# Performance work log

Hardware: AMD Instinct MI355X
Metric: run time of the kernel (lower is better)

Reference implementation:

```python
import jax, jax.numpy as jnp
from jax import lax
import numpy as np

EPS = 1e-5


def fps(xyz, npoint):
    # farthest point sampling, starts at index 0 (pointnet2 convention). xyz: (B,N,3)
    B, N, _ = xyz.shape
    def step(carry, _):
        dist, last = carry
        lastp = jnp.take_along_axis(xyz, last[:, None, None], axis=1)  # (B,1,3)
        d2 = jnp.sum((xyz - lastp) ** 2, axis=-1)                      # (B,N)
        dist = jnp.minimum(dist, d2)
        nxt = jnp.argmax(dist, axis=-1).astype(jnp.int32)
        return (dist, nxt), last
    init = (jnp.full((B, N), 1e10, xyz.dtype), jnp.zeros((B,), jnp.int32))
    _, idxs = lax.scan(step, init, None, length=npoint)
    return jnp.transpose(idxs)  # (B, npoint)


def gather2(x, idx):
    # x (B,N,C), idx (B,S) -> (B,S,C)
    return jnp.take_along_axis(x, idx[..., None], axis=1)


def gather3(x, idx):
    # x (B,N,C), idx (B,S,K) -> (B,S,K,C)
    return jnp.take_along_axis(x[:, None], idx[..., None], axis=2)


def ball_query(xyz, new_xyz, radius, nsample):
    # first nsample indices (in original point order) within radius; pad with first hit
    d2 = jnp.sum((new_xyz[:, :, None, :] - xyz[:, None, :, :]) ** 2, axis=-1)  # (B,S,N)
    N = xyz.shape[1]
    mask = d2 < radius * radius
    cand = jnp.where(mask, jnp.arange(N, dtype=jnp.int32), N)
    cand = jnp.sort(cand, axis=-1)[..., :nsample]
    first = cand[..., :1]
    cand = jnp.where(cand == N, first, cand)
    return jnp.where(cand == N, 0, cand)


def shared_mlp(h, layers):
    # h: (B,S,K,C); 1x1 conv == per-point linear; BN2d with batch stats; ReLU
    for W, g, b in layers:
        h = jnp.einsum('bskc,cd->bskd', h, W)
        mu = jnp.mean(h, axis=(0, 1, 2))
        var = jnp.var(h, axis=(0, 1, 2))
        h = jax.nn.relu((h - mu) * lax.rsqrt(var + EPS) * g + b)
    return h


def sa_module(xyz, feat, npoint, radius, nsample, layers):
    if npoint is None:  # group-all
        grouped = jnp.concatenate([xyz, feat], axis=-1)[:, None]  # (B,1,N,3+C)
        new_xyz = xyz[:, :1]
    else:
        cidx = fps(xyz, npoint)
        new_xyz = gather2(xyz, cidx)                              # (B,S,3)
        nidx = ball_query(xyz, new_xyz, radius, nsample)          # (B,S,K)
        gxyz = gather3(xyz, nidx) - new_xyz[:, :, None, :]        # centered xyz
        grouped = jnp.concatenate([gxyz, gather3(feat, nidx)], axis=-1)
    return new_xyz, jnp.max(shared_mlp(grouped, layers), axis=2)  # (B,S,D)


def bn1d_relu(x, g, b):
    mu = jnp.mean(x, axis=0)
    var = jnp.var(x, axis=0)
    return jax.nn.relu((x - mu) * lax.rsqrt(var + EPS) * g + b)


def setup_inputs():
    key = jax.random.key(0)
    ks = jax.random.split(key, 16)
    B, NP, NG = 64, 1024, 256
    inp = {}
    # points in a 0.1-side cube so radius-0.02/0.04 balls contain realistic neighbor counts
    inp['pc'] = jax.random.uniform(ks[0], (B, NP, 3), jnp.float32) * 0.1
    inp['gripper_pc'] = jax.random.uniform(ks[1], (B, NG, 3), jnp.float32) * 0.1
    def conv(k, cin, cout):
        return jax.random.normal(k, (cin, cout), jnp.float32) * (1.0 / np.sqrt(cin))
    specs = {'w1a': (7, 64), 'w1b': (64, 64), 'w1c': (64, 128),
             'w2a': (131, 128), 'w2b': (128, 128), 'w2c': (128, 256),
             'w3a': (259, 256), 'w3b': (256, 256), 'w3c': (256, 512)}
    i = 2
    for name, (cin, cout) in specs.items():
        inp[name] = conv(ks[i], cin, cout); i += 1
        inp['g' + name[1:]] = jnp.ones((cout,), jnp.float32)
        inp['b' + name[1:]] = jnp.zeros((cout,), jnp.float32)
    inp['fw1'] = conv(ks[i], 512, 1024); i += 1
    inp['fb1'] = jnp.zeros((1024,), jnp.float32)
    inp['fg1'] = jnp.ones((1024,), jnp.float32)
    inp['fbb1'] = jnp.zeros((1024,), jnp.float32)
    inp['fw2'] = conv(ks[i], 1024, 1024); i += 1
    inp['fb2'] = jnp.zeros((1024,), jnp.float32)
    inp['fg2'] = jnp.ones((1024,), jnp.float32)
    inp['fbb2'] = jnp.zeros((1024,), jnp.float32)
    inp['hw'] = conv(ks[i], 1024, 1); i += 1
    inp['hb'] = jnp.zeros((1,), jnp.float32)
    return inp


def reference(pc, gripper_pc,
              w1a, g1a, b1a, w1b, g1b, b1b, w1c, g1c, b1c,
              w2a, g2a, b2a, w2b, g2b, b2b, w2c, g2c, b2c,
              w3a, g3a, b3a, w3b, g3b, b3b, w3c, g3c, b3c,
              fw1, fb1, fg1, fbb1, fw2, fb2, fg2, fbb2, hw, hb):
    B, NP, _ = pc.shape
    NG = gripper_pc.shape[1]
    xyz = jnp.concatenate([pc, gripper_pc], axis=1)                       # (B,N,3)
    labels = jnp.concatenate([jnp.ones((B, NP, 1), pc.dtype),
                              jnp.zeros((B, NG, 1), pc.dtype)], axis=1)
    feat = jnp.concatenate([xyz, labels], axis=-1)                        # (B,N,4)
    xyz, feat = sa_module(xyz, feat, 128, 0.02, 64,
                          [(w1a, g1a, b1a), (w1b, g1b, b1b), (w1c, g1c, b1c)])
    xyz, feat = sa_module(xyz, feat, 32, 0.04, 128,
                          [(w2a, g2a, b2a), (w2b, g2b, b2b), (w2c, g2c, b2c)])
    _, feat = sa_module(xyz, feat, None, None, None,
                        [(w3a, g3a, b3a), (w3b, g3b, b3b), (w3c, g3c, b3c)])
    x = feat[:, 0]                                                        # (B,512)
    x = bn1d_relu(x @ fw1 + fb1, fg1, fbb1)
    x = bn1d_relu(x @ fw2 + fb2, fg2, fbb2)
    return x @ hw + hb                                                    # (B,1) logits
```

## Files before the change

### kernel.cpp

```cpp
#include <hip/hip_runtime.h>

#define BN_EPS 1e-5f
#define MFMA_B16(a, b, c) __builtin_amdgcn_mfma_f32_16x16x32_bf16((a), (b), (c), 0, 0, 0)

typedef short s16x8 __attribute__((ext_vector_type(8)));
typedef float f32x4v __attribute__((ext_vector_type(4)));

__device__ __forceinline__ unsigned fenc(float f) {
    unsigned u = __float_as_uint(f);
    return (u & 0x80000000u) ? ~u : (u | 0x80000000u);
}
__device__ __forceinline__ float fdec(unsigned e) {
    unsigned u = (e & 0x80000000u) ? (e ^ 0x80000000u) : ~e;
    return __uint_as_float(u);
}
__device__ __forceinline__ unsigned short f2b(float f) {
    unsigned u = __float_as_uint(f);
    unsigned r = u + 0x7FFFu + ((u >> 16) & 1u);
    return (unsigned short)(r >> 16);
}
__device__ __forceinline__ float b2f(unsigned short h) {
    return __uint_as_float(((unsigned)h) << 16);
}

__device__ __forceinline__ void cmb(float& v, int& i, float ov, int oi) {
    bool t = (ov > v) || ((ov == v) && (oi < i));
    v = t ? ov : v;
    i = t ? oi : i;
}
template<int CTRL>
__device__ __forceinline__ float dppf(float x) {
    return __uint_as_float((unsigned)__builtin_amdgcn_update_dpp(
        0, (int)__float_as_uint(x), CTRL, 0xF, 0xF, true));
}
template<int CTRL>
__device__ __forceinline__ int dppi(int x) {
    return __builtin_amdgcn_update_dpp(0, x, CTRL, 0xF, 0xF, true);
}

__global__ __launch_bounds__(256) void build_xyz_kernel(
    const float* __restrict__ pc, const float* __restrict__ gpc, float* __restrict__ xyz)
{
    int p = blockIdx.x * 256 + threadIdx.x;
    if (p >= 64 * 1280) return;
    int b = p / 1280, i = p % 1280;
    const float* src = (i < 1024) ? (pc + ((size_t)b * 1024 + i) * 3)
                                  : (gpc + ((size_t)b * 256 + (i - 1024)) * 3);
    xyz[(size_t)p * 3 + 0] = src[0];
    xyz[(size_t)p * 3 + 1] = src[1];
    xyz[(size_t)p * 3 + 2] = src[2];
}

__global__ __launch_bounds__(256) void prep_w_kernel(
    const float* __restrict__ w2a, const float* __restrict__ w2b, const float* __restrict__ w2c,
    const float* __restrict__ w1a, const float* __restrict__ w1b, const float* __restrict__ w1c,
    unsigned short* __restrict__ W1Th, unsigned short* __restrict__ W1Tl,
    unsigned short* __restrict__ W2Th, unsigned short* __restrict__ W2Tl,
    unsigned short* __restrict__ W3Th, unsigned short* __restrict__ W3Tl,
    unsigned short* __restrict__ A1Th, unsigned short* __restrict__ A1Tl,
    unsigned short* __restrict__ B1Th, unsigned short* __restrict__ B1Tl,
    unsigned short* __restrict__ C1Th, unsigned short* __restrict__ C1Tl)
{
    int i = blockIdx.x * 256 + threadIdx.x;
    float v = 0.f;
    unsigned short* dh; unsigned short* dl; int j;
    if (i < 20480) {
        int n = i / 160, k = i % 160;
        if (k < 128)       v = w2a[(size_t)(3 + k) * 128 + n];
        else if (k < 131)  v = w2a[(size_t)(k - 128) * 128 + n];
        dh = W1Th; dl = W1Tl; j = i;
    } else if (i < 36864) {
        j = i - 20480;
        int n = j / 128, k = j % 128;
        v = w2b[(size_t)k * 128 + n];
        dh = W2Th; dl = W2Tl;
    } else if (i < 69632) {
        j = i - 36864;
        int n = j / 128, k = j % 128;
        v = w2c[(size_t)k * 256 + n];
        dh = W3Th; dl = W3Tl;
    } else if (i < 71680) {
        j = i - 69632;
        int n = j / 32, k = j % 32;
        if (k < 7) v = w1a[(size_t)k * 64 + n];
        dh = A1Th; dl = A1Tl;
    } else if (i < 75776) {
        j = i - 71680;
        int n = j / 64, k = j % 64;
        v = w1b[(size_t)k * 64 + n];
        dh = B1Th; dl = B1Tl;
    } else if (i < 83968) {
        j = i - 75776;
        int n = j / 64, k = j % 64;
        v = w1c[(size_t)k * 128 + n];
        dh = C1Th; dl = C1Tl;
    } else return;
    unsigned short hi = f2b(v);
    unsigned short lo = f2b(v - b2f(hi));
    dh[j] = hi; dl[j] = lo;
}

__global__ __launch_bounds__(256) void reduce_stats_kernel(
    const float* __restrict__ PS, const float* __restrict__ PQ,
    int nblk, int C, float* __restrict__ osum, float* __restrict__ osq)
{
    __shared__ float rs_[256], rq_[256];
    int c = blockIdx.x, t = threadIdx.x;
    float s = 0.f, q = 0.f;
    for (int i = t; i < nblk; i += 256) {
        s += PS[(size_t)i * C + c];
        q += PQ[(size_t)i * C + c];
    }
    rs_[t] = s; rq_[t] = q;
    __syncthreads();
    for (int off = 128; off >= 1; off >>= 1) {
        if (t < off) { rs_[t] += rs_[t + off]; rq_[t] += rq_[t + off]; }
        __syncthreads();
    }
    if (t == 0) { osum[c] = rs_[0]; osq[c] = rq_[0]; }
}

template<int P>
__global__ __launch_bounds__(256, 1) void fps_mw_kernel(
    const float* __restrict__ xyz, int N, int S, int* __restrict__ oidx)
{
    __shared__ float sx[1280 * 3];
    __shared__ float rv[2][4];
    __shared__ int   ri[2][4];
    int b = blockIdx.x, t = threadIdx.x;
    int wv = t >> 6, lane = t & 63;
    for (int i = t; i < N * 3; i += 256) sx[i] = xyz[(size_t)b * N * 3 + i];
    __syncthreads();
    float px[P], py[P], pz[P], dm[P];
    #pragma unroll
    for (int p = 0; p < P; p++) {
        int i = t * P + p;
        px[p] = sx[i * 3]; py[p] = sx[i * 3 + 1]; pz[p] = sx[i * 3 + 2];
        dm[p] = 1e10f;
    }
    int last = 0;
    float lx = sx[0], ly = sx[1], lz = sx[2];
    for (int j = 0; j < S; j++) {
        if (t == 0) oidx[b * S + j] = last;
        float bestv = -1.f; int besti = 0;
        #pragma unroll
        for (int p = 0; p < P; p++) {
            float dx = px[p] - lx, dy = py[p] - ly, dz = pz[p] - lz;
            float d2 = __fadd_rn(__fadd_rn(__fmul_rn(dx, dx), __fmul_rn(dy, dy)), __fmul_rn(dz, dz));
            float d = fminf(dm[p], d2); dm[p] = d;
            if (d > bestv) { bestv = d; besti = t * P + p; }
        }
        cmb(bestv, besti, dppf<0xB1>(bestv),  dppi<0xB1>(besti));
        cmb(bestv, besti, dppf<0x4E>(bestv),  dppi<0x4E>(besti));
        cmb(bestv, besti, dppf<0x141>(bestv), dppi<0x141>(besti));
        cmb(bestv, besti, dppf<0x140>(bestv), dppi<0x140>(besti));
        cmb(bestv, besti, __shfl_xor(bestv, 16, 64), __shfl_xor(besti, 16, 64));
        cmb(bestv, besti, __shfl_xor(bestv, 32, 64), __shfl_xor(besti, 32, 64));
        if (lane == 0) { rv[j & 1][wv] = bestv; ri[j & 1][wv] = besti; }
        __syncthreads();
        float bv = rv[j & 1][0]; int bi = ri[j & 1][0];
        cmb(bv, bi, rv[j & 1][1], ri[j & 1][1]);
        cmb(bv, bi, rv[j & 1][2], ri[j & 1][2]);
        cmb(bv, bi, rv[j & 1][3], ri[j & 1][3]);
        last = bi;
        lx = sx[last * 3]; ly = sx[last * 3 + 1]; lz = sx[last * 3 + 2];
    }
}

template<int P>
__global__ __launch_bounds__(64, 1) void fps_wave_kernel(
    const float* __restrict__ xyz, int N, int S, int* __restrict__ oidx)
{
    __shared__ float sx[1280 * 3];
    int b = blockIdx.x, lane = threadIdx.x;
    for (int i = lane; i < N * 3; i += 64) sx[i] = xyz[(size_t)b * N * 3 + i];
    __syncthreads();
    float px[P], py[P], pz[P], dm[P];
    #pragma unroll
    for (int p = 0; p < P; p++) {
        int i = lane * P + p;
        px[p] = sx[i * 3]; py[p] = sx[i * 3 + 1]; pz[p] = sx[i * 3 + 2];
        dm[p] = 1e10f;
    }
    int last = 0;
    float lx = sx[0], ly = sx[1], lz = sx[2];
    for (int j = 0; j < S; j++) {
        if (lane == 0) oidx[b * S + j] = last;
        float bv0 = -1.f, bv1 = -1.f; int bi0 = 0, bi1 = 0;
        #pragma unroll
        for (int p = 0; p < P; p++) {
            float dx = px[p] - lx, dy = py[p] - ly, dz = pz[p] - lz;
            float d2 = __fadd_rn(__fadd_rn(__fmul_rn(dx, dx), __fmul_rn(dy, dy)), __fmul_rn(dz, dz));
            float d = fminf(dm[p], d2); dm[p] = d;
            if (p & 1) { if (d > bv1) { bv1 = d; bi1 = lane * P + p; } }
            else       { if (d > bv0) { bv0 = d; bi0 = lane * P + p; } }
        }
        float bestv = bv0; int besti = bi0;
        cmb(bestv, besti, bv1, bi1);
        cmb(bestv, besti, dppf<0xB1>(bestv),  dppi<0xB1>(besti));
        cmb(bestv, besti, dppf<0x4E>(bestv),  dppi<0x4E>(besti));
        cmb(bestv, besti, dppf<0x141>(bestv), dppi<0x141>(besti));
        cmb(bestv, besti, dppf<0x140>(bestv), dppi<0x140>(besti));
        cmb(bestv, besti, __shfl_xor(bestv, 16, 64), __shfl_xor(besti, 16, 64));
        cmb(bestv, besti, __shfl_xor(bestv, 32, 64), __shfl_xor(besti, 32, 64));
        last = besti;
        lx = sx[last * 3]; ly = sx[last * 3 + 1]; lz = sx[last * 3 + 2];
    }
}

__global__ __launch_bounds__(256) void ball_query_kernel(
    const float* __restrict__ xyz, const int* __restrict__ cidx,
    int N, int S, int nsample, float r2,
    int* __restrict__ nidx, float* __restrict__ newxyz)
{
    __shared__ float sx[1280 * 3];
    int b = blockIdx.x, t = threadIdx.x;
    for (int i = t; i < N * 3; i += 256) sx[i] = xyz[(size_t)b * N * 3 + i];
    __syncthreads();
    int w = t >> 6, lane = t & 63;
    int s = blockIdx.y * 4 + w;
    if (s >= S) return;
    int c = cidx[b * S + s];
    float cx = sx[c * 3], cy = sx[c * 3 + 1], cz = sx[c * 3 + 2];
    if (lane == 0) {
        newxyz[((size_t)b * S + s) * 3 + 0] = cx;
        newxyz[((size_t)b * S + s) * 3 + 1] = cy;
        newxyz[((size_t)b * S + s) * 3 + 2] = cz;
    }
    int P = N >> 6;
    int base = lane * P;
    unsigned mask = 0;
    for (int p = 0; p < P; p++) {
        int i = base + p;
        float dx = sx[i * 3] - cx, dy = sx[i * 3 + 1] - cy, dz = sx[i * 3 + 2] - cz;
        float d2 = __fadd_rn(__fadd_rn(__fmul_rn(dx, dx), __fmul_rn(dy, dy)), __fmul_rn(dz, dz));
        if (d2 < r2) mask |= (1u << p);
    }
    int cnt = __popc(mask);
    int pre = cnt;
    for (int off = 1; off < 64; off <<= 1) {
        int v = __shfl_up(pre, off, 64);
        if (lane >= off) pre += v;
    }
    int excl = pre - cnt;
    int total = __shfl(pre, 63, 64);
    size_t outb = ((size_t)b * S + s) * (size_t)nsample;
    unsigned mm = mask; int pos = excl;
    while (mm) {
        int p = __ffs(mm) - 1; mm &= mm - 1;
        if (pos < nsample) nidx[outb + pos] = base + p;
        pos++;
    }
    unsigned long long bal = __ballot(cnt > 0);
    int firstlane = __ffsll(bal) - 1;
    int firstidx = base + __ffs(mask) - 1;
    firstidx = __shfl(firstidx, firstlane, 64);
    for (int p = total + lane; p < nsample; p += 64) nidx[outb + p] = firstidx;
}

__global__ __launch_bounds__(256) void sa1_moment_kernel(
    const float* __restrict__ xyz, const int* __restrict__ nidx,
    const float* __restrict__ nx, float* __restrict__ mom)
{
    float a[35];
    #pragma unroll
    for (int i = 0; i < 35; i++) a[i] = 0.f;
    int gid = blockIdx.x * 256 + threadIdx.x;
    for (int ch = 0; ch < 8; ch++) {
        int r = ch * 65536 + gid;
        int n = nidx[r];
        int bs = r >> 6, b = r >> 13;
        const float* p = xyz + ((size_t)b * 1280 + n) * 3;
        float cx = nx[bs * 3], cy = nx[bs * 3 + 1], cz = nx[bs * 3 + 2];
        float x[7];
        x[0] = p[0] - cx; x[1] = p[1] - cy; x[2] = p[2] - cz;
        x[3] = p[0]; x[4] = p[1]; x[5] = p[2];
        x[6] = (n < 1024) ? 1.f : 0.f;
        #pragma unroll
        for (int k = 0; k < 7; k++) a[k] += x[k];
        int idx = 7;
        #pragma unroll
        for (int k = 0; k < 7; k++)
            #pragma unroll
            for (int l = k; l < 7; l++) { a[idx] = fmaf(x[k], x[l], a[idx]); idx++; }
    }
    #pragma unroll
    for (int off = 32; off > 0; off >>= 1)
        #pragma unroll
        for (int i = 0; i < 35; i++) a[i] += __shfl_xor(a[i], off, 64);
    __shared__ float red[4][35];
    int wv = threadIdx.x >> 6, lane = threadIdx.x & 63;
    if (lane == 0) {
        #pragma unroll
        for (int i = 0; i < 35; i++) red[wv][i] = a[i];
    }
    __syncthreads();
    int t = threadIdx.x;
    if (t < 35) atomicAdd(&mom[t], red[0][t] + red[1][t] + red[2][t] + red[3][t]);
}

__global__ __launch_bounds__(64) void sa1_mom_fin_kernel(
    const float* __restrict__ mom, const float* __restrict__ w1a,
    float* __restrict__ osum, float* __restrict__ osq)
{
    int n = threadIdx.x;
    float wn[7];
    #pragma unroll
    for (int k = 0; k < 7; k++) wn[k] = w1a[(size_t)k * 64 + n];
    float s = 0.f;
    #pragma unroll
    for (int k = 0; k < 7; k++) s = fmaf(mom[k], wn[k], s);
    float q = 0.f;
    int idx = 7;
    #pragma unroll
    for (int k = 0; k < 7; k++)
        #pragma unroll
        for (int l = k; l < 7; l++) {
            float w2 = wn[k] * wn[l];
            q = fmaf(mom[idx], (k == l) ? w2 : 2.f * w2, q);
            idx++;
        }
    osum[n] = s; osq[n] = q;
}

__global__ __launch_bounds__(256, 4) void sa1_ab_kernel(
    const float* __restrict__ xyz, const int* __restrict__ nidx,
    const float* __restrict__ nx,
    const unsigned short* __restrict__ W1h, const unsigned short* __restrict__ W1l,
    const unsigned short* __restrict__ W2h, const unsigned short* __restrict__ W2l,
    const float* __restrict__ s1, const float* __restrict__ q1,
    const float* __restrict__ g1, const float* __restrict__ b1,
    float* __restrict__ ps, float* __restrict__ pq, float* __restrict__ Y)
{
    __shared__ unsigned short Xhi[64 * 40], Xlo[64 * 40];
    __shared__ unsigned short Hh[64 * 72], Hl[64 * 72];
    __shared__ float aA[64], aB[64];
    __shared__ float cs[64], cq[64];
    const float IR = 1.f / 524288.f;
    int bs = blockIdx.x, b = bs >> 7, t = threadIdx.x;
    if (t < 64) {
        float mu = s1[t] * IR;
        float rs = rsqrtf(q1[t] * IR - mu * mu + BN_EPS);
        float a = rs * g1[t];
        aA[t] = a; aB[t] = b1[t] - mu * a;
        int n = nidx[(size_t)bs * 64 + t];
        const float* p = xyz + ((size_t)b * 1280 + n) * 3;
        float cx = nx[bs * 3], cy = nx[bs * 3 + 1], cz = nx[bs * 3 + 2];
        float v[7] = { p[0] - cx, p[1] - cy, p[2] - cz, p[0], p[1], p[2], (n < 1024) ? 1.f : 0.f };
        #pragma unroll
        for (int k = 0; k < 7; k++) {
            unsigned short hi = f2b(v[k]);
            Xhi[t * 40 + k] = hi;
            Xlo[t * 40 + k] = f2b(v[k] - b2f(hi));
        }
        for (int k = 7; k < 40; k++) { Xhi[t * 40 + k] = 0; Xlo[t * 40 + k] = 0; }
    }
    __syncthreads();
    int wv = t >> 6, lane = t & 63;
    int quad = lane >> 4, l16 = lane & 15;
    int aoff = quad * 8;

    f32x4v acc[4] = {};
    {
        size_t woff = (size_t)(wv * 16 + l16) * 32 + aoff;
        s16x8 bh = *(const s16x8*)(W1h + woff);
        s16x8 bl = *(const s16x8*)(W1l + woff);
        #pragma unroll
        for (int mt = 0; mt < 4; mt++) {
            s16x8 ah = *(const s16x8*)&Xhi[(mt * 16 + l16) * 40 + aoff];
            s16x8 al = *(const s16x8*)&Xlo[(mt * 16 + l16) * 40 + aoff];
            acc[mt] = MFMA_B16(al, bh, acc[mt]);
            acc[mt] = MFMA_B16(ah, bl, acc[mt]);
            acc[mt] = MFMA_B16(ah, bh, acc[mt]);
        }
    }
    {
        int n = wv * 16 + l16;
        float a = aA[n], bb = aB[n];
        #pragma unroll
        for (int mt = 0; mt < 4; mt++)
            #pragma unroll
            for (int r = 0; r < 4; r++) {
                int m = mt * 16 + quad * 4 + r;
                float h = fmaxf(acc[mt][r] * a + bb, 0.f);
                unsigned short hi = f2b(h);
                Hh[m * 72 + n] = hi;
                Hl[m * 72 + n] = f2b(h - b2f(hi));
            }
    }
    __syncthreads();

    f32x4v ac2[4] = {};
    #pragma unroll
    for (int kc = 0; kc < 64; kc += 32) {
        size_t woff = (size_t)(wv * 16 + l16) * 64 + kc + aoff;
        s16x8 bh = *(const s16x8*)(W2h + woff);
        s16x8 bl = *(const s16x8*)(W2l + woff);
        #pragma unroll
        for (int mt = 0; mt < 4; mt++) {
            s16x8 ah = *(const s16x8*)&Hh[(mt * 16 + l16) * 72 + kc + aoff];
            s16x8 al = *(const s16x8*)&Hl[(mt * 16 + l16) * 72 + kc + aoff];
            ac2[mt] = MFMA_B16(al, bh, ac2[mt]);
            ac2[mt] = MFMA_B16(ah, bl, ac2[mt]);
            ac2[mt] = MFMA_B16(ah, bh, ac2[mt]);
        }
    }
    int n = wv * 16 + l16;
    float s = 0.f, q = 0.f;
    #pragma unroll
    for (int mt = 0; mt < 4; mt++)
        #pragma unroll
        for (int r = 0; r < 4; r++) {
            int m = mt * 16 + quad * 4 + r;
            float v = ac2[mt][r];
            Y[((size_t)bs * 64 + m) * 64 + n] = v;
            s += v; q += v * v;
        }
    s += __shfl_xor(s, 16, 64); q += __shfl_xor(q, 16, 64);
    s += __shfl_xor(s, 32, 64); q += __shfl_xor(q, 32, 64);
    if (quad == 0) { cs[n] = s; cq[n] = q; }
    __syncthreads();
    if (t < 64) { ps[(size_t)bs * 64 + t] = cs[t]; pq[(size_t)bs * 64 + t] = cq[t]; }
}

__global__ __launch_bounds__(512, 4) void sa1_c_kernel(
    const float* __restrict__ Y,
    const unsigned short* __restrict__ Wh, const unsigned short* __restrict__ Wl,
    const float* __restrict__ s2, const float* __restrict__ q2,
    const float* __restrict__ g2, const float* __restrict__ b2,
    float* __restrict__ ps, float* __restrict__ pq,
    float* __restrict__ pmax, float* __restrict__ pmin)
{
    __shared__ unsigned short Xhi[128 * 72], Xlo[128 * 72];
    __shared__ float aA[64], aB[64];
    __shared__ float cs2[2][128], cq2[2][128];
    __shared__ float cmx[2][128], cmn[2][128];
    const float IR = 1.f / 524288.f;
    int bs0 = blockIdx.x * 2;
    size_t rbase = (size_t)blockIdx.x * 128;
    int t = threadIdx.x;
    if (t < 64) {
        float mu = s2[t] * IR;
        float rs = rsqrtf(q2[t] * IR - mu * mu + BN_EPS);
        float a = rs * g2[t];
        aA[t] = a; aB[t] = b2[t] - mu * a;
    }
    __syncthreads();
    {
        int r = t >> 2, seg = t & 3;
        const float4* y4 = (const float4*)(Y + (rbase + r) * 64 + seg * 16);
        float4 v[4];
        #pragma unroll
        for (int i = 0; i < 4; i++) v[i] = y4[i];
        s16x8 ph[2], pl[2];
        #pragma unroll
        for (int i = 0; i < 4; i++) {
            #pragma unroll
            for (int j = 0; j < 4; j++) {
                int e = i * 4 + j;
                int c = seg * 16 + e;
                float x = fmaxf(((const float*)&v[i])[j] * aA[c] + aB[c], 0.f);
                unsigned short hi = f2b(x);
                ph[e >> 3][e & 7] = (short)hi;
                pl[e >> 3][e & 7] = (short)f2b(x - b2f(hi));
            }
        }
        #pragma unroll
        for (int k = 0; k < 2; k++) {
            *(s16x8*)&Xhi[r * 72 + seg * 16 + k * 8] = ph[k];
            *(s16x8*)&Xlo[r * 72 + seg * 16 + k * 8] = pl[k];
        }
    }
    __syncthreads();
    int wv = t >> 6, lane = t & 63;
    int wh = wv >> 2, wc = wv & 3;
    int quad = lane >> 4, l16 = lane & 15;
    int aoff = quad * 8;

    f32x4v a3[4][2] = {};
    #pragma unroll
    for (int kc = 0; kc < 64; kc += 32) {
        s16x8 ah[4], al[4];
        #pragma unroll
        for (int mi = 0; mi < 4; mi++) {
            int mt = wh * 4 + mi;
            ah[mi] = *(const s16x8*)&Xhi[(mt * 16 + l16) * 72 + kc + aoff];
            al[mi] = *(const s16x8*)&Xlo[(mt * 16 + l16) * 72 + kc + aoff];
        }
        #pragma unroll
        for (int nt = 0; nt < 2; nt++) {
            size_t woff = (size_t)(wc * 32 + nt * 16 + l16) * 64 + kc + aoff;
            s16x8 bh = *(const s16x8*)(Wh + woff);
            s16x8 bl = *(const s16x8*)(Wl + woff);
            #pragma unroll
            for (int mi = 0; mi < 4; mi++) {
                a3[mi][nt] = MFMA_B16(al[mi], bh, a3[mi][nt]);
                a3[mi][nt] = MFMA_B16(ah[mi], bl, a3[mi][nt]);
                a3[mi][nt] = MFMA_B16(ah[mi], bh, a3[mi][nt]);
            }
        }
    }
    #pragma unroll
    for (int nt = 0; nt < 2; nt++) {
        int n = wc * 32 + nt * 16 + l16;
        float s = 0.f, q = 0.f, mx = -3.4e38f, mn_ = 3.4e38f;
        #pragma unroll
        for (int mi = 0; mi < 4; mi++)
            #pragma unroll
            for (int r = 0; r < 4; r++) {
// ... 692 lines not shown
```

Baseline: 881.3 us.

## Carry winner coordinates through FPS argmax reduction and shorten cross-wave reduction

The FPS kernels now carry the winning point's xyz through the argmax reduction. This removes the dependent LDS lookup of the selected point's coordinates on each serial iteration. In the multi-wave kernel, the two cross-row shuffle stages are replaced by writing 16 per-row partial results to shared memory, which every thread then reduces. The cost is more DPP traffic and more registers per reduction step, plus more LDS reads after the barrier.

Measured after the change: 947.5 us. 7.5% more time.

```diff
diff --git a/kernel.cpp b/kernel.cpp
--- a/kernel.cpp
+++ b/kernel.cpp
@@ -27,6 +27,12 @@
     bool t = (ov > v) || ((ov == v) && (oi < i));
     v = t ? ov : v;
     i = t ? oi : i;
+}
+__device__ __forceinline__ void cmb5(float& v, int& i, float& x, float& y, float& z,
+                                     float ov, int oi, float ox, float oy, float oz) {
+    bool t = (ov > v) || ((ov == v) && (oi < i));
+    v = t ? ov : v; i = t ? oi : i;
+    x = t ? ox : x; y = t ? oy : y; z = t ? oz : z;
 }
 template<int CTRL>
 __device__ __forceinline__ float dppf(float x) {
@@ -125,8 +131,8 @@
     const float* __restrict__ xyz, int N, int S, int* __restrict__ oidx)
 {
     __shared__ float sx[1280 * 3];
-    __shared__ float rv[2][4];
-    __shared__ int   ri[2][4];
+    __shared__ float rv[2][16], rx[2][16], ry[2][16], rz[2][16];
+    __shared__ int   ri[2][16];
     int b = blockIdx.x, t = threadIdx.x;
     int wv = t >> 6, lane = t & 63;
     for (int i = t; i < N * 3; i += 256) sx[i] = xyz[(size_t)b * N * 3 + i];
@@ -137,33 +143,45 @@
         int i = t * P + p;
         px[p] = sx[i * 3]; py[p] = sx[i * 3 + 1]; pz[p] = sx[i * 3 + 2];
         dm[p] = 1e10f;
+        asm volatile("" : "+v"(px[p]), "+v"(py[p]), "+v"(pz[p]));
     }
     int last = 0;
     float lx = sx[0], ly = sx[1], lz = sx[2];
     for (int j = 0; j < S; j++) {
         if (t == 0) oidx[b * S + j] = last;
-        float bestv = -1.f; int besti = 0;
+        float bv = -1.f, bx = 0.f, by = 0.f, bz = 0.f; int bi = 0;
         #pragma unroll
         for (int p = 0; p < P; p++) {
             float dx = px[p] - lx, dy = py[p] - ly, dz = pz[p] - lz;
             float d2 = __fadd_rn(__fadd_rn(__fmul_rn(dx, dx), __fmul_rn(dy, dy)), __fmul_rn(dz, dz));
             float d = fminf(dm[p], d2); dm[p] = d;
-            if (d > bestv) { bestv = d; besti = t * P + p; }
-        }
-        cmb(bestv, besti, dppf<0xB1>(bestv),  dppi<0xB1>(besti));
-        cmb(bestv, besti, dppf<0x4E>(bestv),  dppi<0x4E>(besti));
-        cmb(bestv, besti, dppf<0x141>(bestv), dppi<0x141>(besti));
-        cmb(bestv, besti, dppf<0x140>(bestv), dppi<0x140>(besti));
-        cmb(bestv, besti, __shfl_xor(bestv, 16, 64), __shfl_xor(besti, 16, 64));
-        cmb(bestv, besti, __shfl_xor(bestv, 32, 64), __shfl_xor(besti, 32, 64));
-        if (lane == 0) { rv[j & 1][wv] = bestv; ri[j & 1][wv] = besti; }
+            if (d > bv) { bv = d; bi = t * P + p; bx = px[p]; by = py[p]; bz = pz[p]; }
+        }
+        cmb5(bv, bi, bx, by, bz, dppf<0xB1>(bv),  dppi<0xB1>(bi),  dppf<0xB1>(bx),  dppf<0xB1>(by),  dppf<0xB1>(bz));
+        cmb5(bv, bi, bx, by, bz, dppf<0x4E>(bv),  dppi<0x4E>(bi),  dppf<0x4E>(bx),  dppf<0x4E>(by),  dppf<0x4E>(bz));
+        cmb5(bv, bi, bx, by, bz, dppf<0x141>(bv), dppi<0x141>(bi), dppf<0x141>(bx), dppf<0x141>(by), dppf<0x141>(bz));
+        cmb5(bv, bi, bx, by, bz, dppf<0x140>(bv), dppi<0x140>(bi), dppf<0x140>(bx), dppf<0x140>(by), dppf<0x140>(bz));
+        int buf = j & 1;
+        if ((lane & 15) == 0) {
+            int slot = wv * 4 + (lane >> 4);
+            rv[buf][slot] = bv; ri[buf][slot] = bi;
+            rx[buf][slot] = bx; ry[buf][slot] = by; rz[buf][slot] = bz;
+        }
         __syncthreads();
-        float bv = rv[j & 1][0]; int bi = ri[j & 1][0];
-        cmb(bv, bi, rv[j & 1][1], ri[j & 1][1]);
-        cmb(bv, bi, rv[j & 1][2], ri[j & 1][2]);
-        cmb(bv, bi, rv[j & 1][3], ri[j & 1][3]);
-        last = bi;
-        lx = sx[last * 3]; ly = sx[last * 3 + 1]; lz = sx[last * 3 + 2];
+        float va[16], xa[16], ya[16], za[16]; int ia[16];
+        #pragma unroll
+        for (int k = 0; k < 16; k++) {
+            va[k] = rv[buf][k]; ia[k] = ri[buf][k];
+            xa[k] = rx[buf][k]; ya[k] = ry[buf][k]; za[k] = rz[buf][k];
+        }
+        #pragma unroll
+        for (int st = 8; st >= 1; st >>= 1)
+            #pragma unroll
+            for (int k = 0; k < st; k++)
+                cmb5(va[k], ia[k], xa[k], ya[k], za[k],
+                     va[k + st], ia[k + st], xa[k + st], ya[k + st], za[k + st]);
+        last = ia[0];
+        lx = xa[0]; ly = ya[0]; lz = za[0];
     }
 }
 
@@ -181,30 +199,32 @@
         int i = lane * P + p;
         px[p] = sx[i * 3]; py[p] = sx[i * 3 + 1]; pz[p] = sx[i * 3 + 2];
         dm[p] = 1e10f;
+        asm volatile("" : "+v"(px[p]), "+v"(py[p]), "+v"(pz[p]));
     }
     int last = 0;
     float lx = sx[0], ly = sx[1], lz = sx[2];
     for (int j = 0; j < S; j++) {
         if (lane == 0) oidx[b * S + j] = last;
-        float bv0 = -1.f, bv1 = -1.f; int bi0 = 0, bi1 = 0;
+        float bv = -1.f, bx = 0.f, by = 0.f, bz = 0.f; int bi = 0;
         #pragma unroll
         for (int p = 0; p < P; p++) {
             float dx = px[p] - lx, dy = py[p] - ly, dz = pz[p] - lz;
             float d2 = __fadd_rn(__fadd_rn(__fmul_rn(dx, dx), __fmul_rn(dy, dy)), __fmul_rn(dz, dz));
             float d = fminf(dm[p], d2); dm[p] = d;
-            if (p & 1) { if (d > bv1) { bv1 = d; bi1 = lane * P + p; } }
-            else       { if (d > bv0) { bv0 = d; bi0 = lane * P + p; } }
-        }
-        float bestv = bv0; int besti = bi0;
-        cmb(bestv, besti, bv1, bi1);
-        cmb(bestv, besti, dppf<0xB1>(bestv),  dppi<0xB1>(besti));
-        cmb(bestv, besti, dppf<0x4E>(bestv),  dppi<0x4E>(besti));
-        cmb(bestv, besti, dppf<0x141>(bestv), dppi<0x141>(besti));
-        cmb(bestv, besti, dppf<0x140>(bestv), dppi<0x140>(besti));
-        cmb(bestv, besti, __shfl_xor(bestv, 16, 64), __shfl_xor(besti, 16, 64));
-        cmb(bestv, besti, __shfl_xor(bestv, 32, 64), __shfl_xor(besti, 32, 64));
-        last = besti;
-        lx = sx[last * 3]; ly = sx[last * 3 + 1]; lz = sx[last * 3 + 2];
+            if (d > bv) { bv = d; bi = lane * P + p; bx = px[p]; by = py[p]; bz = pz[p]; }
+        }
+        cmb5(bv, bi, bx, by, bz, dppf<0xB1>(bv),  dppi<0xB1>(bi),  dppf<0xB1>(bx),  dppf<0xB1>(by),  dppf<0xB1>(bz));
+        cmb5(bv, bi, bx, by, bz, dppf<0x4E>(bv),  dppi<0x4E>(bi),  dppf<0x4E>(bx),  dppf<0x4E>(by),  dppf<0x4E>(bz));
+        cmb5(bv, bi, bx, by, bz, dppf<0x141>(bv), dppi<0x141>(bi), dppf<0x141>(bx), dppf<0x141>(by), dppf<0x141>(bz));
+        cmb5(bv, bi, bx, by, bz, dppf<0x140>(bv), dppi<0x140>(bi), dppf<0x140>(bx), dppf<0x140>(by), dppf<0x140>(bz));
+        cmb5(bv, bi, bx, by, bz,
+             __shfl_xor(bv, 16, 64), __shfl_xor(bi, 16, 64),
+             __shfl_xor(bx, 16, 64), __shfl_xor(by, 16, 64), __shfl_xor(bz, 16, 64));
+        cmb5(bv, bi, bx, by, bz,
+             __shfl_xor(bv, 32, 64), __shfl_xor(bi, 32, 64),
+             __shfl_xor(bx, 32, 64), __shfl_xor(by, 32, 64), __shfl_xor(bz, 32, 64));
+        last = bi;
+        lx = bx; ly = by; lz = bz;
     }
 }
 
```
